# Kernel tuning notes

Measured on AMD Instinct MI355X. Metric: run time of the kernel, lower is better.

Reference implementation:

```python
import jax, jax.numpy as jnp
import numpy as np

N = 50000      # nodes
E = 800000     # edges (avg degree 16)
D = 128        # hidden_dim (= in_dim)
H = 8          # heads
DH = D // H    # head dim = 16
L = 2          # num_layers=1 -> ModuleList has 2 layers (extra append)
LN_EPS = 1e-5


def layer_norm(x, w, b):
    m = jnp.mean(x, axis=-1, keepdims=True)
    v = jnp.mean((x - m) ** 2, axis=-1, keepdims=True)
    return (x - m) * jax.lax.rsqrt(v + LN_EPS) * w + b


def setup_inputs() -> dict:
    key = jax.random.key(0)
    ks = jax.random.split(key, 16)
    s = 0.05

    def nrm(k, shape):
        return jax.random.normal(k, shape, jnp.float32) * s

    inp = {
        "h": jax.random.normal(ks[0], (N, D), jnp.float32),
        "src": jax.random.randint(ks[1], (E,), 0, N),
        "dst": jax.random.randint(ks[2], (E,), 0, N),
        "W_emb": nrm(ks[3], (D, D)),
        "Wq": nrm(ks[4], (L, D, D)), "bq": jnp.zeros((L, D), jnp.float32),
        "Wk": nrm(ks[5], (L, D, D)), "bk": jnp.zeros((L, D), jnp.float32),
        "Wv": nrm(ks[6], (L, D, D)), "bv": jnp.zeros((L, D), jnp.float32),
        "Wo": nrm(ks[7], (L, D, D)), "bo": jnp.zeros((L, D), jnp.float32),
        "ln1_w": jnp.ones((L, D), jnp.float32), "ln1_b": jnp.zeros((L, D), jnp.float32),
        "Wf1": nrm(ks[8], (L, D, 2 * D)), "bf1": jnp.zeros((L, 2 * D), jnp.float32),
        "Wf2": nrm(ks[9], (L, 2 * D, D)), "bf2": jnp.zeros((L, D), jnp.float32),
        "ln2_w": jnp.ones((L, D), jnp.float32), "ln2_b": jnp.zeros((L, D), jnp.float32),
    }
    return inp


def reference(h, src, dst, W_emb, Wq, bq, Wk, bk, Wv, bv, Wo, bo,
              ln1_w, ln1_b, Wf1, bf1, Wf2, bf2, ln2_w, ln2_b):
    n = h.shape[0]
    scale = 1.0 / np.sqrt(DH)  # np.sqrt(self.out_dim), out_dim = head dim = 16
    h = h @ W_emb  # embedding_h (no bias)
    for l in range(L):
        q = (h @ Wq[l] + bq[l]).reshape(n, H, DH)
        k = (h @ Wk[l] + bk[l]).reshape(n, H, DH)
        v = (h @ Wv[l] + bv[l]).reshape(n, H, DH)
        # per-edge score: K[src] . Q[dst], scaled, clamped, exponentiated
        s = jnp.einsum('ehd,ehd->eh', k[src], q[dst]) * scale  # [E,H]
        s = jnp.exp(jnp.clip(s, -5.0, 5.0))
        # scatter-sum weighted V and normalizer z into dst nodes
        wV = jax.ops.segment_sum(v[src] * s[:, :, None], dst, num_segments=n)  # [N,H,DH]
        z = jax.ops.segment_sum(s, dst, num_segments=n)                        # [N,H]
        attn = (wV / (z[:, :, None] + 1e-6)).reshape(n, D)
        hx = layer_norm(h + attn @ Wo[l] + bo[l], ln1_w[l], ln1_b[l])
        ffn = jax.nn.relu(hx @ Wf1[l] + bf1[l]) @ Wf2[l] + bf2[l]  # dropout inactive (eval)
        h = layer_norm(hx + ffn, ln2_w[l], ln2_b[l])
    return h
```

## Files before the change

kernel.cpp:

```cpp
#include <hip/hip_runtime.h>
#include <math.h>

static constexpr int N_NODES = 50000;
static constexpr int N_EDGES = 800000;
static constexpr int DMODEL  = 128;
static constexpr int MTILES  = N_NODES / 16;
static constexpr int CAPLOG  = 6;
static constexpr int ESPLIT  = 400384;

typedef __attribute__((ext_vector_type(8))) short short8;
typedef __attribute__((ext_vector_type(4))) float float4v;

__device__ __forceinline__ unsigned short f2bf(float f) {
    unsigned u = __builtin_bit_cast(unsigned, f);
    u += 0x7fffu + ((u >> 16) & 1u);
    return (unsigned short)(u >> 16);
}
__device__ __forceinline__ float bf2f(unsigned short b) {
    unsigned u = ((unsigned)b) << 16;
    return __builtin_bit_cast(float, u);
}

struct PrepSeg { const float* src; int K; int N; int dstOff; };
struct PrepArgs { PrepSeg seg[13]; };

__global__ void prep_kernel(PrepArgs pa, unsigned short* wf, int* counts)
{
    if (blockIdx.y == 13) {
        for (int i = blockIdx.x * 256 + threadIdx.x; i < N_NODES; i += 128 * 256)
            counts[i] = 0;
        return;
    }
    PrepSeg sg = pa.seg[blockIdx.y];
    int e = blockIdx.x * 256 + threadIdx.x;
    int total = sg.K * sg.N;
    if (e >= total) return;
    int n = e % sg.N;
    int k = e / sg.N;
    int ks = sg.K >> 5;
    int nt = n >> 4, c = n & 15, s = k >> 5, q = (k >> 3) & 3, jj = k & 7;
    int di = sg.dstOff + (nt * ks + s) * 512 + q * 128 + c * 8 + jj;
    wf[di] = f2bf(sg.src[e]);
}

__device__ __forceinline__ void scatter_body(
    const int* __restrict__ src, const int* __restrict__ dst,
    int* counts, int* eslot, int ebeg, int eend)
{
    int blk = ebeg + blockIdx.x * 1024;
    if (blk >= eend) return;
    int base = blk + threadIdx.x;
    int d[4], s[4];
    bool v[4];
#pragma unroll
    for (int k = 0; k < 4; ++k) {
        int e = base + k * 256;
        v[k] = e < eend;
        int ec = v[k] ? e : ebeg;
        d[k] = dst[ec];
        s[k] = src[ec];
    }
#pragma unroll
    for (int k = 0; k < 4; ++k) {
        if (v[k]) {
            int r = atomicAdd(&counts[d[k]], 1);
            eslot[(d[k] << CAPLOG) + r] = s[k];
        }
    }
}

template<int KSTEPS, int NT, int EPI, bool AF32, bool WRF, bool WRB>
__device__ __forceinline__ void gemm_body(
    const void* __restrict__ Ap, const unsigned short* __restrict__ Wfc,
    const float* __restrict__ bias, const float* res,
    float* Cf, unsigned short* Cb,
    const float* __restrict__ lnw, const float* __restrict__ lnb,
    int ldA, int ldC, int mtiles, int colBase)
{
    const int lane = threadIdx.x & 63;
    const int c = lane & 15;
    const int q = lane >> 4;

    __shared__ unsigned short smB[NT * KSTEPS * 512];
    {
        const int totalVec = NT * KSTEPS * 64;
        const uint4* gsrc = (const uint4*)Wfc;
        uint4* sdst = (uint4*)smB;
#pragma unroll
        for (int i = threadIdx.x; i < totalVec; i += 256)
            sdst[i] = gsrc[i];
    }
    __syncthreads();

    short8 bfrag[NT][KSTEPS];
#pragma unroll
    for (int nt = 0; nt < NT; ++nt)
#pragma unroll
        for (int s = 0; s < KSTEPS; ++s)
            bfrag[nt][s] = *(const short8*)(smB + (nt * KSTEPS + s) * 512 + lane * 8);

    float bb[NT];
#pragma unroll
    for (int nt = 0; nt < NT; ++nt)
        bb[nt] = bias ? bias[colBase + nt * 16 + c] : 0.f;

    float lw[NT], lb[NT];
    if (EPI == 3) {
#pragma unroll
        for (int nt = 0; nt < NT; ++nt) {
            lw[nt] = lnw[nt * 16 + c];
            lb[nt] = lnb[nt * 16 + c];
        }
    }

    const int wid = blockIdx.x * 4 + (threadIdx.x >> 6);
    const int nw  = gridDim.x * 4;

    for (int mt = wid; mt < mtiles; mt += nw) {
        const int row0 = mt * 16;
        short8 afrag[KSTEPS];
        if (AF32) {
            const float* A32 = (const float*)Ap;
#pragma unroll
            for (int s = 0; s < KSTEPS; ++s) {
                const float4* p = (const float4*)(A32 + (size_t)(row0 + c) * ldA + s * 32 + q * 8);
                float4 x0 = p[0], x1 = p[1];
                short8 a;
                a[0] = (short)f2bf(x0.x); a[1] = (short)f2bf(x0.y);
                a[2] = (short)f2bf(x0.z); a[3] = (short)f2bf(x0.w);
                a[4] = (short)f2bf(x1.x); a[5] = (short)f2bf(x1.y);
                a[6] = (short)f2bf(x1.z); a[7] = (short)f2bf(x1.w);
                afrag[s] = a;
            }
        } else {
            const unsigned short* Ab = (const unsigned short*)Ap;
#pragma unroll
            for (int s = 0; s < KSTEPS; ++s)
                afrag[s] = *(const short8*)(Ab + (size_t)(row0 + c) * ldA + s * 32 + q * 8);
        }

        float4v acc[NT];
#pragma unroll
        for (int nt = 0; nt < NT; ++nt) acc[nt] = (float4v)0.f;
#pragma unroll
        for (int s = 0; s < KSTEPS; ++s)
#pragma unroll
            for (int nt = 0; nt < NT; ++nt)
                acc[nt] = __builtin_amdgcn_mfma_f32_16x16x32_bf16(afrag[s], bfrag[nt][s], acc[nt], 0, 0, 0);

#pragma unroll
        for (int nt = 0; nt < NT; ++nt) {
            const int col = colBase + nt * 16 + c;
#pragma unroll
            for (int r = 0; r < 4; ++r) {
                const int grow = row0 + q * 4 + r;
                float v = acc[nt][r] + bb[nt];
                if (EPI == 2 || EPI == 3) v += res[(size_t)grow * ldC + col];
                if (EPI == 1) v = fmaxf(v, 0.f);
                acc[nt][r] = v;
            }
        }

        if (EPI == 3) {
#pragma unroll
            for (int r = 0; r < 4; ++r) {
                float s = 0.f, ss = 0.f;
#pragma unroll
                for (int nt = 0; nt < NT; ++nt) {
                    float v = acc[nt][r];
                    s += v; ss = fmaf(v, v, ss);
                }
#pragma unroll
                for (int o = 1; o < 16; o <<= 1) {
                    s  += __shfl_xor(s, o, 64);
                    ss += __shfl_xor(ss, o, 64);
                }
                float m   = s * (1.0f / 128.0f);
                float var = ss * (1.0f / 128.0f) - m * m;
                float rs  = rsqrtf(var + 1e-5f);
                const int grow = row0 + q * 4 + r;
#pragma unroll
                for (int nt = 0; nt < NT; ++nt) {
                    float v = (acc[nt][r] - m) * rs * lw[nt] + lb[nt];
                    if (WRF) Cf[(size_t)grow * ldC + nt * 16 + c] = v;
                    if (WRB) Cb[(size_t)grow * ldC + nt * 16 + c] = f2bf(v);
                }
            }
        } else {
#pragma unroll
            for (int nt = 0; nt < NT; ++nt) {
                const int col = colBase + nt * 16 + c;
#pragma unroll
                for (int r = 0; r < 4; ++r) {
                    const int grow = row0 + q * 4 + r;
                    if (WRF) Cf[(size_t)grow * ldC + col] = acc[nt][r];
                    if (WRB) Cb[(size_t)grow * ldC + col] = f2bf(acc[nt][r]);
                }
            }
        }
    }
}

template<int KSTEPS, int NT, int EPI, bool AF32, bool WRF, bool WRB>
__global__ __launch_bounds__(256, 2)
void mfma_gemm(const void* __restrict__ Ap, const unsigned short* __restrict__ Wf,
               const float* __restrict__ bias, const float* res,
               float* Cf, unsigned short* Cb,
               const float* __restrict__ lnw, const float* __restrict__ lnb,
               int ldA, int ldC, int mtiles)
{
    const int colBase = blockIdx.y * NT * 16;
    const unsigned short* Wfc = Wf + (size_t)blockIdx.y * NT * KSTEPS * 512;
    gemm_body<KSTEPS, NT, EPI, AF32, WRF, WRB>(
        Ap, Wfc, bias, res, Cf, Cb, lnw, lnb, ldA, ldC, mtiles, colBase);
}

__global__ __launch_bounds__(256, 2)
void emb_sc_gemm(const float* __restrict__ A, const unsigned short* __restrict__ Wf,
                 float* Cf, unsigned short* Cb, int mtiles,
                 const int* __restrict__ src, const int* __restrict__ dst,
                 int* counts, int* eslot, int ebeg, int eend)
{
    if (blockIdx.y == 1) {
        scatter_body(src, dst, counts, eslot, ebeg, eend);
        return;
    }
    gemm_body<4, 8, 0, true, true, true>(
        A, Wf, nullptr, nullptr, Cf, Cb, nullptr, nullptr, 128, 128, mtiles, 0);
}

struct QkvPtrs { const float* bias[3]; unsigned short* out[3]; int ldc[3]; };

__global__ __launch_bounds__(256, 2)
void qkv_sc_gemm(const unsigned short* __restrict__ A, const unsigned short* __restrict__ WfBase,
                 QkvPtrs ptrs, int mtiles,
                 const int* __restrict__ src, const int* __restrict__ dst,
                 int* counts, int* eslot, int ebeg, int eend)
{
    if (blockIdx.y == 3) {
        scatter_body(src, dst, counts, eslot, ebeg, eend);
        return;
    }
    const int sel = blockIdx.y;
    gemm_body<4, 8, 0, false, false, true>(
        A, WfBase + (size_t)sel * 32768, ptrs.bias[sel], nullptr,
        nullptr, ptrs.out[sel], nullptr, nullptr, 128, ptrs.ldc[sel], mtiles, 0);
}

template<bool WRB>
__global__ __launch_bounds__(256, 2)
void ffn_kernel(const unsigned short* __restrict__ A,
                const unsigned short* __restrict__ W1,
                const unsigned short* __restrict__ W2,
                const float* __restrict__ b1, const float* __restrict__ b2,
                const float* __restrict__ res,
                float* Cf, unsigned short* Cb,
                const float* __restrict__ lnw, const float* __restrict__ lnb,
                int mtiles)
{
    const int lane = threadIdx.x & 63;
    const int c = lane & 15;
    const int q = lane >> 4;
    const int w = threadIdx.x >> 6;

    __shared__ unsigned short exf[8 * 64 * 8];
    __shared__ float sred[16][4][2];

    short8 b1f[4][4];
#pragma unroll
    for (int nt = 0; nt < 4; ++nt)
#pragma unroll
        for (int s = 0; s < 4; ++s)
            b1f[nt][s] = *(const short8*)(W1 + (size_t)((w * 4 + nt) * 4 + s) * 512 + lane * 8);

    short8 b2f[2][8];
#pragma unroll
    for (int nt = 0; nt < 2; ++nt)
#pragma unroll
        for (int s = 0; s < 8; ++s)
            b2f[nt][s] = *(const short8*)(W2 + (size_t)((w * 2 + nt) * 8 + s) * 512 + lane * 8);

    float bb1[4];
#pragma unroll
    for (int nt = 0; nt < 4; ++nt) bb1[nt] = b1[w * 64 + nt * 16 + c];
    float bb2[2], lw[2], lb[2];
#pragma unroll
    for (int nt = 0; nt < 2; ++nt) {
        int col = w * 32 + nt * 16 + c;
        bb2[nt] = b2[col]; lw[nt] = lnw[col]; lb[nt] = lnb[col];
    }

    const int iters = (mtiles + gridDim.x - 1) / gridDim.x;
    for (int it = 0; it < iters; ++it) {
        const int mt = blockIdx.x + it * gridDim.x;
        const bool active = mt < mtiles;
        const int row0 = (active ? mt : 0) * 16;

        short8 af[4];
#pragma unroll
        for (int s = 0; s < 4; ++s)
            af[s] = *(const short8*)(A + (size_t)(row0 + c) * 128 + s * 32 + q * 8);

        float4v acc1[4];
#pragma unroll
        for (int nt = 0; nt < 4; ++nt) acc1[nt] = (float4v)0.f;
#pragma unroll
        for (int s = 0; s < 4; ++s)
#pragma unroll
            for (int nt = 0; nt < 4; ++nt)
                acc1[nt] = __builtin_amdgcn_mfma_f32_16x16x32_bf16(af[s], b1f[nt][s], acc1[nt], 0, 0, 0);

#pragma unroll
        for (int nt = 0; nt < 4; ++nt) {
            const int col = w * 64 + nt * 16 + c;
            const int base = ((col >> 5) * 4 + ((col >> 3) & 3)) * 16;
            const int j = col & 7;
#pragma unroll
            for (int r = 0; r < 4; ++r) {
                float v = fmaxf(acc1[nt][r] + bb1[nt], 0.f);
                exf[(size_t)(base + q * 4 + r) * 8 + j] = f2bf(v);
            }
        }
        __syncthreads();

        short8 af2[8];
#pragma unroll
        for (int s = 0; s < 8; ++s)
            af2[s] = *(const short8*)(exf + (size_t)(s * 64 + lane) * 8);

        float4v acc2[2];
#pragma unroll
        for (int nt = 0; nt < 2; ++nt) acc2[nt] = (float4v)0.f;
#pragma unroll
        for (int s = 0; s < 8; ++s)
#pragma unroll
            for (int nt = 0; nt < 2; ++nt)
                acc2[nt] = __builtin_amdgcn_mfma_f32_16x16x32_bf16(af2[s], b2f[nt][s], acc2[nt], 0, 0, 0);

        float vv[2][4];
#pragma unroll
        for (int nt = 0; nt < 2; ++nt)
#pragma unroll
            for (int r = 0; r < 4; ++r)
                vv[nt][r] = acc2[nt][r] + bb2[nt] +
                            res[(size_t)(row0 + q * 4 + r) * 128 + w * 32 + nt * 16 + c];

#pragma unroll
        for (int r = 0; r < 4; ++r) {
            float s  = vv[0][r] + vv[1][r];
            float ss = fmaf(vv[0][r], vv[0][r], vv[1][r] * vv[1][r]);
#pragma unroll
            for (int o = 1; o < 16; o <<= 1) {
                s  += __shfl_xor(s, o, 64);
                ss += __shfl_xor(ss, o, 64);
            }
            if (c == 0) {
                sred[q * 4 + r][w][0] = s;
                sred[q * 4 + r][w][1] = ss;
            }
        }
        __syncthreads();

#pragma unroll
        for (int r = 0; r < 4; ++r) {
            const int rr = q * 4 + r;
            float S  = sred[rr][0][0] + sred[rr][1][0] + sred[rr][2][0] + sred[rr][3][0];
            float SS = sred[rr][0][1] + sred[rr][1][1] + sred[rr][2][1] + sred[rr][3][1];
            float m   = S * (1.0f / 128.0f);
            float var = SS * (1.0f / 128.0f) - m * m;
            float rs  = rsqrtf(var + 1e-5f);
            if (active) {
                const int grow = row0 + rr;
#pragma unroll
                for (int nt = 0; nt < 2; ++nt) {
                    const int col = w * 32 + nt * 16 + c;
                    float v = (vv[nt][r] - m) * rs * lw[nt] + lb[nt];
                    Cf[(size_t)grow * 128 + col] = v;
                    if (WRB) Cb[(size_t)grow * 128 + col] = f2bf(v);
                }
            }
        }
    }
}

__global__ __launch_bounds__(256)
void agg_kernel(const unsigned short* qv, const unsigned short* __restrict__ kvv,
                const int* __restrict__ counts, const int* __restrict__ eslot,
                unsigned short* attn, int n_nodes)
{
    int w    = (int)((blockIdx.x * 256 + threadIdx.x) >> 6);
    int lane = threadIdx.x & 63;
    if (w >= n_nodes) return;
    const int g  = lane >> 4;
    const int li = lane & 15;

    float qf[8];
    {
        uint4 qb = *(const uint4*)(qv + (size_t)w * 128 + li * 8);
        const unsigned* qp = (const unsigned*)&qb;
#pragma unroll
        for (int j = 0; j < 4; ++j) {
            qf[2 * j]     = bf2f((unsigned short)(qp[j] & 0xffff));
            qf[2 * j + 1] = bf2f((unsigned short)(qp[j] >> 16));
        }
    }

    const int beg = w << CAPLOG;
    const int end = beg + counts[w];
    float acc[8] = {0.f, 0.f, 0.f, 0.f, 0.f, 0.f, 0.f, 0.f};
    float z = 0.f;

    for (int e = beg; e < end; e += 8) {
        int  i0 = e + g;
        int  i1 = e + g + 4;
        bool v0 = i0 < end;
        bool v1 = i1 < end;
        int  s0 = eslot[v0 ? i0 : beg];
        int  s1 = eslot[v1 ? i1 : beg];

        const unsigned short* b0 = kvv + (size_t)s0 * 256 + li * 8;
        const unsigned short* b1 = kvv + (size_t)s1 * 256 + li * 8;
        uint4 kb0 = *(const uint4*)(b0);
        uint4 vb0 = *(const uint4*)(b0 + 128);
        uint4 kb1 = *(const uint4*)(b1);
        uint4 vb1 = *(const uint4*)(b1 + 128);

        const unsigned* kp0 = (const unsigned*)&kb0;
        const unsigned* kp1 = (const unsigned*)&kb1;
        float p0 = 0.f, p1 = 0.f;
#pragma unroll
        for (int j = 0; j < 4; ++j) {
            p0 = fmaf(bf2f((unsigned short)(kp0[j] & 0xffff)), qf[2 * j],     p0);
            p0 = fmaf(bf2f((unsigned short)(kp0[j] >> 16)),    qf[2 * j + 1], p0);
            p1 = fmaf(bf2f((unsigned short)(kp1[j] & 0xffff)), qf[2 * j],     p1);
            p1 = fmaf(bf2f((unsigned short)(kp1[j] >> 16)),    qf[2 * j + 1], p1);
        }
        p0 += __shfl_xor(p0, 1, 64);
        p1 += __shfl_xor(p1, 1, 64);

        float sv0 = __expf(fminf(fmaxf(p0 * 0.25f, -5.f), 5.f));
        float sv1 = __expf(fminf(fmaxf(p1 * 0.25f, -5.f), 5.f));
        sv0 = v0 ? sv0 : 0.f;
        sv1 = v1 ? sv1 : 0.f;

        const unsigned* vp0 = (const unsigned*)&vb0;
        const unsigned* vp1 = (const unsigned*)&vb1;
#pragma unroll
        for (int j = 0; j < 4; ++j) {
            acc[2 * j]     = fmaf(sv0, bf2f((unsigned short)(vp0[j] & 0xffff)), acc[2 * j]);
            acc[2 * j + 1] = fmaf(sv0, bf2f((unsigned short)(vp0[j] >> 16)),    acc[2 * j + 1]);
            acc[2 * j]     = fmaf(sv1, bf2f((unsigned short)(vp1[j] & 0xffff)), acc[2 * j]);
            acc[2 * j + 1] = fmaf(sv1, bf2f((unsigned short)(vp1[j] >> 16)),    acc[2 * j + 1]);
        }
        z += sv0 + sv1;
    }

#pragma unroll
    for (int o = 16; o < 64; o <<= 1) {
#pragma unroll
        for (int j = 0; j < 8; ++j) acc[j] += __shfl_xor(acc[j], o, 64);
        z += __shfl_xor(z, o, 64);
    }

    if (g == 0) {
        float inv = 1.f / (z + 1e-6f);
        unsigned ow[4];
#pragma unroll
        for (int j = 0; j < 4; ++j)
            ow[j] = (unsigned)f2bf(acc[2 * j] * inv) |
                    ((unsigned)f2bf(acc[2 * j + 1] * inv) << 16);
        *(uint4*)(attn + (size_t)w * 128 + li * 8) = *(const uint4*)ow;
    }
}

extern "C" void kernel_launch(void* const* d_in, const int* in_sizes, int n_in,
                              void* d_out, int out_size, void* d_ws, size_t ws_size,
                              hipStream_t stream)
{
    const float* h_in  = (const float*)d_in[0];
    const int*   src   = (const int*)d_in[1];
    const int*   dst   = (const int*)d_in[2];
    const float* W_emb = (const float*)d_in[3];
    const float* Wq    = (const float*)d_in[4];
    const float* bq    = (const float*)d_in[5];
    const float* Wk    = (const float*)d_in[6];
    const float* bk    = (const float*)d_in[7];
    const float* Wv    = (const float*)d_in[8];
    const float* bv    = (const float*)d_in[9];
    const float* Wo    = (const float*)d_in[10];
    const float* bo    = (const float*)d_in[11];
    const float* ln1w  = (const float*)d_in[12];
    const float* ln1b  = (const float*)d_in[13];
    const float* Wf1   = (const float*)d_in[14];
    const float* bf1   = (const float*)d_in[15];
    const float* Wf2   = (const float*)d_in[16];
    const float* bf2   = (const float*)d_in[17];
    const float* ln2w  = (const float*)d_in[18];
    const float* ln2b  = (const float*)d_in[19];
    float* out = (float*)d_out;

    const int N = N_NODES, E = N_EDGES;
    const size_t NF = (size_t)N * DMODEL;

    float*          hbuf  = (float*)d_ws;
    unsigned short* hbf   = (unsigned short*)(hbuf + NF);
    unsigned short* qbuf  = hbf + NF;
    unsigned short* kvbuf = qbuf + NF;
    unsigned short* wf    = kvbuf + 2 * NF;
    int* counts = (int*)(wf + 278528);
    int* eslot  = (int*)d_out;

    const int EMB_O = 0, Q_O = 16384, K_O = 49152, V_O = 81920, O_O = 114688,
              F1_O = 147456, F2_O = 212992;

    const int GX = 391;

    PrepArgs pa;
    pa.seg[0]  = {W_emb,          128, 128, EMB_O};
    pa.seg[1]  = {Wq,             128, 128, Q_O};
    pa.seg[2]  = {Wq + 16384,     128, 128, Q_O + 16384};
    pa.seg[3]  = {Wk,             128, 128, K_O};
    pa.seg[4]  = {Wk + 16384,     128, 128, K_O + 16384};
    pa.seg[5]  = {Wv,             128, 128, V_O};
    pa.seg[6]  = {Wv + 16384,     128, 128, V_O + 16384};
    pa.seg[7]  = {Wo,             128, 128, O_O};
    pa.seg[8]  = {Wo + 16384,     128, 128, O_O + 16384};
    pa.seg[9]  = {Wf1,            128, 256, F1_O};
    pa.seg[10] = {Wf1 + 32768,    128, 256, F1_O + 32768};
    pa.seg[11] = {Wf2,            256, 128, F2_O};
    pa.seg[12] = {Wf2 + 32768,    256, 128, F2_O + 32768};
    prep_kernel<<<dim3(128, 14), 256, 0, stream>>>(pa, wf, counts);

    emb_sc_gemm<<<dim3(GX, 2), 256, 0, stream>>>(
        h_in, wf + EMB_O, hbuf, hbf, MTILES, src, dst, counts, eslot, 0, ESPLIT);

    const int rowBlocks = (N + 3) / 4;
    for (int l = 0; l < 2; ++l) {
        QkvPtrs qp;
        qp.bias[0] = bq + l * 128; qp.bias[1] = bk + l * 128; qp.bias[2] = bv + l * 128;
        qp.out[0] = qbuf;   qp.ldc[0] = 128;
        qp.out[1] = kvbuf;  qp.ldc[1] = 256;
        qp.out[2] = kvbuf + 128; qp.ldc[2] = 256;
        qkv_sc_gemm<<<dim3(GX, l == 0 ? 4 : 3), 256, 0, stream>>>(
            hbf, wf + Q_O + l * 16384, qp, MTILES, src, dst, counts, eslot,
            l == 0 ? ESPLIT : 0, l == 0 ? E : 0);

        agg_kernel<<<rowBlocks, 256, 0, stream>>>(qbuf, kvbuf, counts, eslot, qbuf, N);

        mfma_gemm<4, 8, 3, false, true, true><<<dim3(GX, 1), 256, 0, stream>>>(
            qbuf, wf + O_O + l * 16384, bo + l * 128, hbuf, hbuf, hbf,
            ln1w + l * 128, ln1b + l * 128, 128, 128, MTILES);

        if (l == 0)
            ffn_kernel<true><<<dim3(GX, 1), 256, 0, stream>>>(
                hbf, wf + F1_O, wf + F2_O, bf1, bf2,
                hbuf, hbuf, hbf, ln2w, ln2b, MTILES);
        else
            ffn_kernel<false><<<dim3(GX, 1), 256, 0, stream>>>(
                hbf, wf + F1_O + 32768, wf + F2_O + 32768, bf1 + 256, bf2 + 128,
                hbuf, out, nullptr, ln2w + 128, ln2b + 128, MTILES);
    }
}
```

Measured before the change: 394.7 us.

## Fuse output projection and first LayerNorm into the FFN block kernel

Merges the attention output projection, residual add and LayerNorm1 into the FFN kernel. The normalized hx stays in registers and shared memory instead of being written to and read back from global memory in fp32 and bf16. This removes one kernel launch per layer and a full round trip of the hidden state. In exchange the fused kernel holds more weight fragments in registers (W0 added), which may lower occupancy, and it adds extra barriers per tile.

```diff
diff --git a/kernel.cpp b/kernel.cpp
--- a/kernel.cpp
+++ b/kernel.cpp
@@ -201,20 +201,6 @@
     }
 }
 
-template<int KSTEPS, int NT, int EPI, bool AF32, bool WRF, bool WRB>
-__global__ __launch_bounds__(256, 2)
-void mfma_gemm(const void* __restrict__ Ap, const unsigned short* __restrict__ Wf,
-               const float* __restrict__ bias, const float* res,
-               float* Cf, unsigned short* Cb,
-               const float* __restrict__ lnw, const float* __restrict__ lnb,
-               int ldA, int ldC, int mtiles)
-{
-    const int colBase = blockIdx.y * NT * 16;
-    const unsigned short* Wfc = Wf + (size_t)blockIdx.y * NT * KSTEPS * 512;
-    gemm_body<KSTEPS, NT, EPI, AF32, WRF, WRB>(
-        Ap, Wfc, bias, res, Cf, Cb, lnw, lnb, ldA, ldC, mtiles, colBase);
-}
-
 __global__ __launch_bounds__(256, 2)
 void emb_sc_gemm(const float* __restrict__ A, const unsigned short* __restrict__ Wf,
                  float* Cf, unsigned short* Cb, int mtiles,
@@ -249,13 +235,16 @@
 
 template<bool WRB>
 __global__ __launch_bounds__(256, 2)
-void ffn_kernel(const unsigned short* __restrict__ A,
+void blk_kernel(const unsigned short* __restrict__ attn,
+                const unsigned short* __restrict__ W0,
                 const unsigned short* __restrict__ W1,
                 const unsigned short* __restrict__ W2,
+                const float* __restrict__ b0,
                 const float* __restrict__ b1, const float* __restrict__ b2,
+                const float* __restrict__ l1wv, const float* __restrict__ l1bv,
+                const float* __restrict__ l2wv, const float* __restrict__ l2bv,
                 const float* __restrict__ res,
                 float* Cf, unsigned short* Cb,
-                const float* __restrict__ lnw, const float* __restrict__ lnb,
                 int mtiles)
 {
     const int lane = threadIdx.x & 63;
@@ -263,8 +252,17 @@
     const int q = lane >> 4;
     const int w = threadIdx.x >> 6;
 
+    __shared__ unsigned short hxf[4 * 64 * 8];
     __shared__ unsigned short exf[8 * 64 * 8];
-    __shared__ float sred[16][4][2];
+    __shared__ float sred1[16][4][2];
+    __shared__ float sred2[16][4][2];
+
+    short8 b0f[2][4];
+#pragma unroll
+    for (int nt = 0; nt < 2; ++nt)
+#pragma unroll
+        for (int s = 0; s < 4; ++s)
+            b0f[nt][s] = *(const short8*)(W0 + (size_t)((w * 2 + nt) * 4 + s) * 512 + lane * 8);
 
     short8 b1f[4][4];
 #pragma unroll
@@ -280,15 +278,16 @@
         for (int s = 0; s < 8; ++s)
             b2f[nt][s] = *(const short8*)(W2 + (size_t)((w * 2 + nt) * 8 + s) * 512 + lane * 8);
 
-    float bb1[4];
-#pragma unroll
-    for (int nt = 0; nt < 4; ++nt) bb1[nt] = b1[w * 64 + nt * 16 + c];
-    float bb2[2], lw[2], lb[2];
+    float bb0[2], l1w[2], l1b[2], bb2[2], l2w[2], l2b[2];
 #pragma unroll
     for (int nt = 0; nt < 2; ++nt) {
         int col = w * 32 + nt * 16 + c;
-        bb2[nt] = b2[col]; lw[nt] = lnw[col]; lb[nt] = lnb[col];
-    }
+        bb0[nt] = b0[col];  l1w[nt] = l1wv[col]; l1b[nt] = l1bv[col];
+        bb2[nt] = b2[col];  l2w[nt] = l2wv[col]; l2b[nt] = l2bv[col];
+    }
+    float bb1[4];
+#pragma unroll
+    for (int nt = 0; nt < 4; ++nt) bb1[nt] = b1[w * 64 + nt * 16 + c];
 
     const int iters = (mtiles + gridDim.x - 1) / gridDim.x;
     for (int it = 0; it < iters; ++it) {
@@ -296,10 +295,72 @@
         const bool active = mt < mtiles;
         const int row0 = (active ? mt : 0) * 16;
 
-        short8 af[4];
+        short8 af0[4];
 #pragma unroll
         for (int s = 0; s < 4; ++s)
-            af[s] = *(const short8*)(A + (size_t)(row0 + c) * 128 + s * 32 + q * 8);
+            af0[s] = *(const short8*)(attn + (size_t)(row0 + c) * 128 + s * 32 + q * 8);
+
+        float4v acc0[2];
+#pragma unroll
+        for (int nt = 0; nt < 2; ++nt) acc0[nt] = (float4v)0.f;
+#pragma unroll
+        for (int s = 0; s < 4; ++s)
+#pragma unroll
+            for (int nt = 0; nt < 2; ++nt)
+                acc0[nt] = __builtin_amdgcn_mfma_f32_16x16x32_bf16(af0[s], b0f[nt][s], acc0[nt], 0, 0, 0);
+
+        float vv0[2][4];
+#pragma unroll
+        for (int nt = 0; nt < 2; ++nt)
+#pragma unroll
+            for (int r = 0; r < 4; ++r)
+                vv0[nt][r] = acc0[nt][r] + bb0[nt] +
+                             res[(size_t)(row0 + q * 4 + r) * 128 + w * 32 + nt * 16 + c];
+
+#pragma unroll
+        for (int r = 0; r < 4; ++r) {
+            float s  = vv0[0][r] + vv0[1][r];
+            float ss = fmaf(vv0[0][r], vv0[0][r], vv0[1][r] * vv0[1][r]);
+#pragma unroll
+            for (int o = 1; o < 16; o <<= 1) {
+                s  += __shfl_xor(s, o, 64);
+                ss += __shfl_xor(ss, o, 64);
+            }
+            if (c == 0) {
+                sred1[q * 4 + r][w][0] = s;
+                sred1[q * 4 + r][w][1] = ss;
+            }
+        }
+        __syncthreads();
+
+        float hx[2][4];
+#pragma unroll
+        for (int r = 0; r < 4; ++r) {
+            const int rr = q * 4 + r;
+            float S  = sred1[rr][0][0] + sred1[rr][1][0] + sred1[rr][2][0] + sred1[rr][3][0];
+            float SS = sred1[rr][0][1] + sred1[rr][1][1] + sred1[rr][2][1] + sred1[rr][3][1];
+            float m   = S * (1.0f / 128.0f);
+            float var = SS * (1.0f / 128.0f) - m * m;
+            float rs  = rsqrtf(var + 1e-5f);
+#pragma unroll
+            for (int nt = 0; nt < 2; ++nt)
+                hx[nt][r] = (vv0[nt][r] - m) * rs * l1w[nt] + l1b[nt];
+        }
+#pragma unroll
+        for (int nt = 0; nt < 2; ++nt) {
+            const int col = w * 32 + nt * 16 + c;
+            const int base = ((col >> 5) * 4 + ((col >> 3) & 3)) * 16;
+            const int j = col & 7;
+#pragma unroll
+            for (int r = 0; r < 4; ++r)
+                hxf[(size_t)(base + q * 4 + r) * 8 + j] = f2bf(hx[nt][r]);
+        }
+        __syncthreads();
+
+        short8 af1[4];
+#pragma unroll
+        for (int s = 0; s < 4; ++s)
+            af1[s] = *(const short8*)(hxf + (size_t)(s * 64 + lane) * 8);
 
         float4v acc1[4];
 #pragma unroll
@@ -308,7 +369,7 @@
         for (int s = 0; s < 4; ++s)
 #pragma unroll
             for (int nt = 0; nt < 4; ++nt)
-                acc1[nt] = __builtin_amdgcn_mfma_f32_16x16x32_bf16(af[s], b1f[nt][s], acc1[nt], 0, 0, 0);
+                acc1[nt] = __builtin_amdgcn_mfma_f32_16x16x32_bf16(af1[s], b1f[nt][s], acc1[nt], 0, 0, 0);
 
 #pragma unroll
         for (int nt = 0; nt < 4; ++nt) {
@@ -337,26 +398,25 @@
             for (int nt = 0; nt < 2; ++nt)
                 acc2[nt] = __builtin_amdgcn_mfma_f32_16x16x32_bf16(af2[s], b2f[nt][s], acc2[nt], 0, 0, 0);
 
-        float vv[2][4];
+        float vv2[2][4];
 #pragma unroll
         for (int nt = 0; nt < 2; ++nt)
 #pragma unroll
             for (int r = 0; r < 4; ++r)
-                vv[nt][r] = acc2[nt][r] + bb2[nt] +
-                            res[(size_t)(row0 + q * 4 + r) * 128 + w * 32 + nt * 16 + c];
+                vv2[nt][r] = acc2[nt][r] + bb2[nt] + hx[nt][r];
 
 #pragma unroll
         for (int r = 0; r < 4; ++r) {
-            float s  = vv[0][r] + vv[1][r];
-            float ss = fmaf(vv[0][r], vv[0][r], vv[1][r] * vv[1][r]);
+            float s  = vv2[0][r] + vv2[1][r];
+            float ss = fmaf(vv2[0][r], vv2[0][r], vv2[1][r] * vv2[1][r]);
 #pragma unroll
             for (int o = 1; o < 16; o <<= 1) {
                 s  += __shfl_xor(s, o, 64);
                 ss += __shfl_xor(ss, o, 64);
             }
             if (c == 0) {
-                sred[q * 4 + r][w][0] = s;
-                sred[q * 4 + r][w][1] = ss;
+                sred2[q * 4 + r][w][0] = s;
+                sred2[q * 4 + r][w][1] = ss;
             }
         }
         __syncthreads();
@@ -364,8 +424,8 @@
 #pragma unroll
         for (int r = 0; r < 4; ++r) {
             const int rr = q * 4 + r;
-            float S  = sred[rr][0][0] + sred[rr][1][0] + sred[rr][2][0] + sred[rr][3][0];
-            float SS = sred[rr][0][1] + sred[rr][1][1] + sred[rr][2][1] + sred[rr][3][1];
+            float S  = sred2[rr][0][0] + sred2[rr][1][0] + sred2[rr][2][0] + sred2[rr][3][0];
+            float SS = sred2[rr][0][1] + sred2[rr][1][1] + sred2[rr][2][1] + sred2[rr][3][1];
             float m   = S * (1.0f / 128.0f);
             float var = SS * (1.0f / 128.0f) - m * m;
             float rs  = rsqrtf(var + 1e-5f);
@@ -374,7 +434,7 @@
 #pragma unroll
                 for (int nt = 0; nt < 2; ++nt) {
                     const int col = w * 32 + nt * 16 + c;
-                    float v = (vv[nt][r] - m) * rs * lw[nt] + lb[nt];
+                    float v = (vv2[nt][r] - m) * rs * l2w[nt] + l2b[nt];
                     Cf[(size_t)grow * 128 + col] = v;
                     if (WRB) Cb[(size_t)grow * 128 + col] = f2bf(v);
                 }
@@ -547,17 +607,15 @@
 
         agg_kernel<<<rowBlocks, 256, 0, stream>>>(qbuf, kvbuf, counts, eslot, qbuf, N);
 
-        mfma_gemm<4, 8, 3, false, true, true><<<dim3(GX, 1), 256, 0, stream>>>(
-            qbuf, wf + O_O + l * 16384, bo + l * 128, hbuf, hbuf, hbf,
-            ln1w + l * 128, ln1b + l * 128, 128, 128, MTILES);
-
         if (l == 0)
-            ffn_kernel<true><<<dim3(GX, 1), 256, 0, stream>>>(
-                hbf, wf + F1_O, wf + F2_O, bf1, bf2,
-                hbuf, hbuf, hbf, ln2w, ln2b, MTILES);
+            blk_kernel<true><<<dim3(GX, 1), 256, 0, stream>>>(
+                qbuf, wf + O_O, wf + F1_O, wf + F2_O,
+                bo, bf1, bf2, ln1w, ln1b, ln2w, ln2b,
+                hbuf, hbuf, hbf, MTILES);
         else
-            ffn_kernel<false><<<dim3(GX, 1), 256, 0, stream>>>(
-                hbf, wf + F1_O + 32768, wf + F2_O + 32768, bf1 + 256, bf2 + 128,
-                hbuf, out, nullptr, ln2w + 128, ln2b + 128, MTILES);
-    }
-}
+            blk_kernel<false><<<dim3(GX, 1), 256, 0, stream>>>(
+                qbuf, wf + O_O + 16384, wf + F1_O + 32768, wf + F2_O + 32768,
+                bo + 128, bf1 + 256, bf2 + 128, ln1w + 128, ln1b + 128,
+                ln2w + 128, ln2b + 128, hbuf, out, nullptr, MTILES);
+    }
+}
```

After: 385.1 us. -2.4%, faster.
